# Kernel optimization log

Hardware: AMD Instinct MI355X
Metric: run time of the kernel (lower is better)

The kernel has to match this reference:

```python
import jax, jax.numpy as jnp
import numpy as np

# dims: batch B, seq T, model C, expert hidden H, num experts E, top-k K
B, T, C, H, E, K = 4, 1024, 1024, 1024, 8, 2


def _swiglu(x):
    a, b = jnp.split(x, 2, axis=-1)
    return jax.nn.silu(a) * b


def setup_inputs() -> dict:
    key = jax.random.key(0)
    ks = jax.random.split(key, 6)
    s = 0.02
    x = jax.random.normal(ks[0], (B, T, C), jnp.float32)
    # weights stored [in, out] (transpose of torch Linear layout; same math y = x @ W)
    w_shared_in = jax.random.normal(ks[1], (C, 2 * H), jnp.float32) * s
    w_shared_out = jax.random.normal(ks[2], (H, C), jnp.float32) * s
    w1_shared = jax.random.normal(ks[3], (C, 2 * H), jnp.float32) * s
    w2 = jax.random.normal(ks[4], (E, H, C), jnp.float32) * s  # stacked routed_w2
    w_gate = jax.random.normal(ks[5], (C, E), jnp.float32) * s
    gate_bias = jnp.zeros((E,), jnp.float32)  # buffer, updated only in training
    return {
        "x": x,
        "w_shared_in": w_shared_in,
        "w_shared_out": w_shared_out,
        "w1_shared": w1_shared,
        "w2": w2,
        "w_gate": w_gate,
        "gate_bias": gate_bias,
    }


def reference(x, w_shared_in, w_shared_out, w1_shared, w2, w_gate, gate_bias):
    Bx, Tx, Cx = x.shape
    S = Bx * Tx
    fx = x.reshape(S, Cx)  # [S, C]

    # shared expert: SwiGLU MLP
    shared_out = _swiglu(fx @ w_shared_in) @ w_shared_out  # [S, C]

    # router: softmax(top-k) over biased logits
    logits = fx @ w_gate + gate_bias  # [S, E]
    probs = jax.nn.softmax(logits, axis=-1)
    top_val, top_idx = jax.lax.top_k(probs, K)  # [S, K]

    # dense dispatch-weight matrix [S, E] (zero where expert not selected)
    wdense = jnp.zeros((S, E), probs.dtype).at[
        jnp.arange(S)[:, None], top_idx
    ].add(top_val)

    # routed experts share w1_shared, so the SwiGLU hidden is identical for all
    # experts; compute it once for every token, then apply per-expert w2.
    hid = _swiglu(fx @ w1_shared)  # [S, H]
    routed_out = jnp.zeros_like(shared_out)
    for e in range(E):  # small fixed expert count
        routed_out = routed_out + wdense[:, e:e + 1] * (hid @ w2[e])

    return (shared_out + routed_out).reshape(Bx, Tx, Cx)
```

## Files before the change

kernel.cpp:

```cpp
#include <hip/hip_runtime.h>
#include <stdint.h>

typedef __attribute__((ext_vector_type(4))) float f32x4;
typedef __attribute__((ext_vector_type(8))) short s16x8;

static constexpr int S_TOK = 4096;
static constexpr int CDIM  = 1024;
static constexpr int HDIM  = 1024;
static constexpr int H2    = 2048;
static constexpr int NEXP  = 8;

#define MAXRT2 40

__device__ __forceinline__ unsigned short f2bf(float f) {
  union { float f; uint32_t u; } c; c.f = f;
  uint32_t u = c.u;
  u += 0x7fffu + ((u >> 16) & 1u);
  return (unsigned short)(u >> 16);
}

__device__ __forceinline__ float bf2f(unsigned short u) {
  return __uint_as_float(((uint32_t)u) << 16);
}

__device__ __forceinline__ void gload16(const void* g, void* l) {
  __builtin_amdgcn_global_load_lds(
      (const __attribute__((address_space(1))) void*)g,
      (__attribute__((address_space(3))) void*)l, 16, 0, 0);
}

__global__ void cast_bf16_kernel(const float* __restrict__ src,
                                 unsigned short* __restrict__ dst, int n4) {
  int i = blockIdx.x * blockDim.x + threadIdx.x;
  const int st = gridDim.x * blockDim.x;
  for (; i < n4; i += st) {
    float4 v = reinterpret_cast<const float4*>(src)[i];
    ushort4 o;
    o.x = f2bf(v.x); o.y = f2bf(v.y); o.z = f2bf(v.z); o.w = f2bf(v.w);
    reinterpret_cast<ushort4*>(dst)[i] = o;
  }
}

__global__ void wprep_in_kernel(const float* __restrict__ wsi, const float* __restrict__ w1s,
                                unsigned short* __restrict__ dst) {
  __shared__ float t[32][33];
  const float* src = blockIdx.z ? w1s : wsi;
  const int halfoff = blockIdx.z ? 2048 : 0;
  const int r0 = blockIdx.y * 32;
  const int c0 = blockIdx.x * 32;
  const int tid = threadIdx.x;
#pragma unroll
  for (int i = 0; i < 4; ++i) {
    int idx = tid + i * 256;
    int r = idx >> 5, c = idx & 31;
    t[r][c] = src[(size_t)(r0 + r) * H2 + c0 + c];
  }
  __syncthreads();
#pragma unroll
  for (int i = 0; i < 4; ++i) {
    int idx = tid + i * 256;
    int r = idx >> 5, c = idx & 31;
    const int ccol = c0 + r;
    const int part = ccol >> 10, h = ccol & 1023;
    const int drow = halfoff + (h & 15) + ((h >> 4) << 5) + (part << 4);
    dst[(size_t)drow * CDIM + r0 + c] = f2bf(t[c][r]);
  }
}

__global__ void transpose_cast_kernel(const float* __restrict__ src,
                                      unsigned short* __restrict__ dst,
                                      int R, int Cc) {
  __shared__ float t[32][33];
  const size_t zoff = (size_t)blockIdx.z * R * Cc;
  src += zoff; dst += zoff;
  const int r0 = blockIdx.y * 32;
  const int c0 = blockIdx.x * 32;
  const int tid = threadIdx.x;
#pragma unroll
  for (int i = 0; i < 4; ++i) {
    int idx = tid + i * 256;
    int r = idx >> 5, c = idx & 31;
    t[r][c] = src[(size_t)(r0 + r) * Cc + c0 + c];
  }
  __syncthreads();
#pragma unroll
  for (int i = 0; i < 4; ++i) {
    int idx = tid + i * 256;
    int r = idx >> 5, c = idx & 31;
    dst[(size_t)(c0 + r) * R + r0 + c] = f2bf(t[c][r]);
  }
}

__global__ void router_kernel(const float* __restrict__ x, const float* __restrict__ wg,
                              const float* __restrict__ gb,
                              int2* __restrict__ ti_e, float2* __restrict__ ti_w) {
  const int l = threadIdx.x & 63;
  const int wid = threadIdx.x >> 6;
  const int s = blockIdx.x * 4 + wid;
  const float* xr = x + (size_t)s * CDIM;
  float acc[NEXP];
#pragma unroll
  for (int e = 0; e < NEXP; ++e) acc[e] = 0.f;
  for (int c = l; c < CDIM; c += 64) {
    float xv = xr[c];
    const float* wr_ = wg + (size_t)c * NEXP;
#pragma unroll
    for (int e = 0; e < NEXP; ++e) acc[e] += xv * wr_[e];
  }
#pragma unroll
  for (int e = 0; e < NEXP; ++e) {
#pragma unroll
    for (int off = 32; off > 0; off >>= 1) acc[e] += __shfl_xor(acc[e], off);
    acc[e] += gb[e];
  }
  float m = acc[0];
#pragma unroll
  for (int e = 1; e < NEXP; ++e) m = fmaxf(m, acc[e]);
  float ex[NEXP], sum = 0.f;
#pragma unroll
  for (int e = 0; e < NEXP; ++e) { ex[e] = __expf(acc[e] - m); sum += ex[e]; }
  int i0 = 0;
#pragma unroll
  for (int e = 1; e < NEXP; ++e) if (acc[e] > acc[i0]) i0 = e;
  int i1 = (i0 == 0) ? 1 : 0;
#pragma unroll
  for (int e = 0; e < NEXP; ++e) {
    if (e == i0) continue;
    if (acc[e] > acc[i1]) i1 = e;
  }
  if (l == 0) {
    const float inv = 1.f / sum;
    ti_e[s] = make_int2(i0, i1);
    ti_w[s] = make_float2(ex[i0] * inv, ex[i1] * inv);
  }
}

__global__ __launch_bounds__(1024) void build_kernel(
    const int2* __restrict__ ti_e,
    int* __restrict__ cnt, int* __restrict__ offs,
    int* __restrict__ gidx, int2* __restrict__ ti_slot) {
  __shared__ int gcnt[64][NEXP];
  __shared__ int gbase[64][NEXP];
  __shared__ int eoff[NEXP];
  const int tid = threadIdx.x;
  const int wid = tid >> 6, lane = tid & 63;

  for (int p = 0; p < 4; ++p) {
    const int g = p * 16 + wid;
    const int2 e = ti_e[g * 64 + lane];
#pragma unroll
    for (int ex = 0; ex < NEXP; ++ex) {
      uint64_t b0 = __ballot(e.x == ex);
      uint64_t b1 = __ballot(e.y == ex);
      if (lane == 0) gcnt[g][ex] = __popcll(b0) + __popcll(b1);
    }
  }
  __syncthreads();
  if (tid < NEXP) {
    const int ex = tid;
    int a = 0;
    for (int g = 0; g < 64; ++g) { gbase[g][ex] = a; a += gcnt[g][ex]; }
    eoff[ex] = a;
  }
  __syncthreads();
  if (tid == 0) {
    int a = 0;
#pragma unroll
    for (int ex = 0; ex < NEXP; ++ex) {
      const int c = eoff[ex];
      offs[ex] = a; cnt[ex] = c; eoff[ex] = a; a += c;
    }
    offs[NEXP] = a;
  }
  __syncthreads();
  for (int p = 0; p < 4; ++p) {
    const int g = p * 16 + wid;
    const int s = g * 64 + lane;
    const int2 e = ti_e[s];
    const uint64_t below = (lane == 0) ? 0ull : (~0ull >> (64 - lane));
    const uint64_t beloweq = below | (1ull << lane);
    int slot0 = 0, slot1 = 0;
#pragma unroll
    for (int ex = 0; ex < NEXP; ++ex) {
      uint64_t b0 = __ballot(e.x == ex);
      uint64_t b1 = __ballot(e.y == ex);
      const int base = gbase[g][ex];
      if (e.x == ex) slot0 = base + __popcll(b0 & below) + __popcll(b1 & below);
      if (e.y == ex) slot1 = base + __popcll(b0 & beloweq) + __popcll(b1 & below);
    }
    ti_slot[s] = make_int2(slot0, slot1);
    gidx[eoff[e.x] + slot0] = s;
    gidx[eoff[e.y] + slot1] = s;
  }
}


template<bool LAST>
__device__ __forceinline__ void iter8(
    const unsigned short* a00, const unsigned short* a01,
    const unsigned short* a10, const unsigned short* a11,
    const unsigned short* b00, const unsigned short* b01,
    const unsigned short* b10, const unsigned short* b11,
    unsigned short* SA, unsigned short* SB,
    int e, int t8, int awb, int bwb, int ak0, int ak1,
    f32x4 (&acc)[8][4]) {
  const int o = e + 1;
  s16x8 a[4][2], bl[2][2], bh[2][2];

#define LD_A4(d, F0) { _Pragma("unroll") for (int f_ = 0; f_ < 4; ++f_) { \
    const unsigned short* p_ = SA + (d) * 16384 + awb + ((F0) + f_) * 1024; \
    a[f_][0] = *reinterpret_cast<const s16x8*>(p_ + ak0); \
    a[f_][1] = *reinterpret_cast<const s16x8*>(p_ + ak1); } }
#define LD_B2(d, bb, N0) { _Pragma("unroll") for (int n_ = 0; n_ < 2; ++n_) { \
    const unsigned short* p_ = SB + (d) * 16384 + bwb + ((N0) + n_) * 1024; \
    bb[n_][0] = *reinterpret_cast<const s16x8*>(p_ + ak0); \
    bb[n_][1] = *reinterpret_cast<const s16x8*>(p_ + ak1); } }
#define STG2(S, d, h, p0, p1, kt) { \
    gload16((p0) + (size_t)(kt) * 64, (S) + (d) * 16384 + (h) * 8192 + t8); \
    gload16((p1) + (size_t)(kt) * 64, (S) + (d) * 16384 + (h) * 8192 + 4096 + t8); }
#define QUAD(F0, bb, N0) { _Pragma("unroll") for (int k_ = 0; k_ < 2; ++k_) \
    { _Pragma("unroll") for (int f_ = 0; f_ < 4; ++f_) \
      { _Pragma("unroll") for (int n_ = 0; n_ < 2; ++n_) \
        acc[(F0) + f_][(N0) + n_] = __builtin_amdgcn_mfma_f32_16x16x32_bf16( \
            a[f_][k_], bb[n_][k_], acc[(F0) + f_][(N0) + n_], 0, 0, 0); } } }
#define PH_MID() { asm volatile("" ::: "memory"); __builtin_amdgcn_s_barrier(); \
    asm volatile("s_waitcnt lgkmcnt(0)" ::: "memory"); __builtin_amdgcn_s_setprio(1); }
#define PH_END() { __builtin_amdgcn_s_setprio(0); asm volatile("" ::: "memory"); \
    __builtin_amdgcn_s_barrier(); asm volatile("" ::: "memory"); }

  LD_A4(0, 0) LD_B2(0, bl, 0)
  STG2(SA, 1, 0, a00, a01, o) STG2(SA, 1, 1, a10, a11, o)
  PH_MID() QUAD(0, bl, 0) PH_END()
  LD_B2(0, bh, 2)
  PH_MID() QUAD(0, bh, 2) PH_END()
  LD_A4(0, 4)
  if (!LAST) STG2(SB, 0, 0, b00, b01, e + 2)
  PH_MID() QUAD(4, bh, 2) PH_END()
  if (!LAST) {
    STG2(SB, 0, 1, b10, b11, e + 2)
    asm volatile("s_waitcnt vmcnt(4)" ::: "memory");
  } else {
    asm volatile("s_waitcnt vmcnt(0)" ::: "memory");
  }
  PH_MID() QUAD(4, bl, 0) PH_END()
  LD_A4(1, 0) LD_B2(1, bl, 0)
  if (!LAST) STG2(SA, 0, 0, a00, a01, e + 2)
  PH_MID() QUAD(0, bl, 0) PH_END()
  LD_B2(1, bh, 2)
  if (!LAST) STG2(SA, 0, 1, a10, a11, e + 2)
  PH_MID() QUAD(0, bh, 2) PH_END()
  LD_A4(1, 4)
  if (!LAST) STG2(SB, 1, 0, b00, b01, o + 2)
  PH_MID() QUAD(4, bh, 2) PH_END()
  if (!LAST) {
    STG2(SB, 1, 1, b10, b11, o + 2)
    asm volatile("s_waitcnt vmcnt(4)" ::: "memory");
  }
  PH_MID() QUAD(4, bl, 0) PH_END()

#undef LD_A4
#undef LD_B2
#undef STG2
#undef QUAD
#undef PH_MID
#undef PH_END
}

__device__ __forceinline__ void prologue8(
    const unsigned short* a00, const unsigned short* a01,
    const unsigned short* a10, const unsigned short* a11,
    const unsigned short* b00, const unsigned short* b01,
    const unsigned short* b10, const unsigned short* b11,
    unsigned short* SA, unsigned short* SB, int t8) {
  gload16(a00, SA + t8);                gload16(a01, SA + 4096 + t8);
  gload16(a10, SA + 8192 + t8);         gload16(a11, SA + 8192 + 4096 + t8);
  gload16(b00, SB + t8);                gload16(b01, SB + 4096 + t8);
  gload16(b10, SB + 8192 + t8);         gload16(b11, SB + 8192 + 4096 + t8);
  gload16(b00 + 64, SB + 16384 + t8);   gload16(b01 + 64, SB + 16384 + 4096 + t8);
  gload16(b10 + 64, SB + 16384 + 8192 + t8);
  gload16(b11 + 64, SB + 16384 + 8192 + 4096 + t8);
  asm volatile("s_waitcnt vmcnt(4)" ::: "memory");
  asm volatile("" ::: "memory");
  __builtin_amdgcn_s_barrier();
  asm volatile("" ::: "memory");
}

__global__ __launch_bounds__(512, 2) void gemm1_kernel(
    const unsigned short* __restrict__ xb, const unsigned short* __restrict__ w12i,
    unsigned short* __restrict__ Hs, unsigned short* __restrict__ Hr) {
  __shared__ unsigned short SA[32768];
  __shared__ unsigned short SB[32768];
  const int tid = threadIdx.x;
  const int l = tid & 63, wid = tid >> 6;
  const int wm = wid >> 2, wn = wid & 3;
  const int lr = l & 15;
  const int awb = wm * 8192 + lr * 64;
  const int bwb = wn * 4096 + lr * 64;
  const int ak0 = (((l >> 4) << 3)) ^ ((l & 7) << 3);
  const int ak1 = 32 ^ ak0;
  const int hw = blockIdx.y * gridDim.x + blockIdx.x;
  const int logical = (hw & 7) * 32 + (hw >> 3);
  const int m0 = (logical >> 4) * 256;
  const int n0 = (logical & 15) * 256;
  const int srow = tid >> 3;
  const int scol = (((tid & 7) ^ (srow & 7)) << 3);
  const int t8 = tid * 8;
  f32x4 acc[8][4] = {};
  const unsigned short* a00 = xb + (size_t)(m0 + srow) * CDIM + scol;
  const unsigned short* a01 = a00 + (size_t)64 * CDIM;
  const unsigned short* a10 = a00 + (size_t)128 * CDIM;
  const unsigned short* a11 = a00 + (size_t)192 * CDIM;
  const unsigned short* b00 = w12i + (size_t)(n0 + srow) * CDIM + scol;
  const unsigned short* b01 = b00 + (size_t)64 * CDIM;
  const unsigned short* b10 = b00 + (size_t)128 * CDIM;
  const unsigned short* b11 = b00 + (size_t)192 * CDIM;

  prologue8(a00, a01, a10, a11, b00, b01, b10, b11, SA, SB, t8);
  for (int it = 0; it < 7; ++it)
    iter8<false>(a00, a01, a10, a11, b00, b01, b10, b11, SA, SB, 2 * it,
                 t8, awb, bwb, ak0, ak1, acc);
  iter8<true>(a00, a01, a10, a11, b00, b01, b10, b11, SA, SB, 14,
              t8, awb, bwb, ak0, ak1, acc);

  unsigned short* Hbuf = (n0 < 2048) ? Hs : Hr;
  const int rb = m0 + wm * 128 + ((l >> 4) << 2);
  const int hbase = ((n0 & 2047) >> 1) + wn * 32;
#pragma unroll
  for (int fm = 0; fm < 8; ++fm)
#pragma unroll
    for (int j = 0; j < 2; ++j)
#pragma unroll
      for (int r = 0; r < 4; ++r) {
        float av = acc[fm][2 * j][r];
        float bv = acc[fm][2 * j + 1][r];
        float hv = (av / (1.f + __expf(-av))) * bv;
        Hbuf[(size_t)(rb + fm * 16 + r) * HDIM + hbase + j * 16 + lr] = f2bf(hv);
      }
}

__global__ __launch_bounds__(512, 2) void gemm2_kernel(
    const unsigned short* __restrict__ Hs, const unsigned short* __restrict__ Hr,
    const unsigned short* __restrict__ wso_t, const unsigned short* __restrict__ w2t,
    const int* __restrict__ cnt, const int* __restrict__ offs, const int* __restrict__ gidx,
    unsigned short* __restrict__ Dout, unsigned short* __restrict__ Eout) {
  __shared__ unsigned short SA[32768];
  __shared__ unsigned short SB[32768];
  const int tid = threadIdx.x;
  const int l = tid & 63, wid = tid >> 6;
  const int wm = wid >> 2, wn = wid & 3;
  const int lr = l & 15;
  const int awb = wm * 8192 + lr * 64;
  const int bwb = wn * 4096 + lr * 64;
  const int ak0 = (((l >> 4) << 3)) ^ ((l & 7) << 3);
  const int ak1 = 32 ^ ak0;
  const int hw = blockIdx.y * gridDim.x + blockIdx.x;
  const int logical = (hw & 7) * 28 + (hw >> 3);
  const int gx = logical >> 2;
  const int n0 = (logical & 3) * 256;
  const int srow = tid >> 3;
  const int scol = (((tid & 7) ^ (srow & 7)) << 3);
  const int t8 = tid * 8;
  f32x4 acc[8][4] = {};

  const unsigned short *a00, *a01, *a10, *a11, *b00, *b01, *b10, *b11;
  int e = 0, cnte = 0, mt = 0, base = 0;
  const bool dense = (gx < 16);
  if (dense) {
    const int m0 = gx * 256;
    a00 = Hs + (size_t)(m0 + srow) * HDIM + scol;
    a01 = a00 + (size_t)64 * HDIM;
    a10 = a00 + (size_t)128 * HDIM;
    a11 = a00 + (size_t)192 * HDIM;
    b00 = wso_t + (size_t)(n0 + srow) * HDIM + scol;
    b01 = b00 + (size_t)64 * HDIM;
    b10 = b00 + (size_t)128 * HDIM;
    b11 = b00 + (size_t)192 * HDIM;
  } else {
    int t = gx - 16;
    bool found = false;
#pragma unroll
    for (int ee = 0; ee < NEXP; ++ee) {
      int c = cnt[ee];
      int nt = (c + 255) >> 8;
      if (!found) {
        if (t < nt) { e = ee; cnte = c; found = true; }
        else t -= nt;
      }
    }
    if (!found) return;
    mt = t;
    base = offs[e];
    const int r0 = mt * 256 + srow;
    const int t0 = gidx[base + min(r0,       cnte - 1)];
    const int t1 = gidx[base + min(r0 + 64,  cnte - 1)];
    const int t2 = gidx[base + min(r0 + 128, cnte - 1)];
    const int t3 = gidx[base + min(r0 + 192, cnte - 1)];
    a00 = Hr + (size_t)t0 * HDIM + scol;
    a01 = Hr + (size_t)t1 * HDIM + scol;
    a10 = Hr + (size_t)t2 * HDIM + scol;
    a11 = Hr + (size_t)t3 * HDIM + scol;
    b00 = w2t + (size_t)e * CDIM * HDIM + (size_t)(n0 + srow) * HDIM + scol;
    b01 = b00 + (size_t)64 * HDIM;
    b10 = b00 + (size_t)128 * HDIM;
    b11 = b00 + (size_t)192 * HDIM;
  }

  prologue8(a00, a01, a10, a11, b00, b01, b10, b11, SA, SB, t8);
  for (int it = 0; it < 7; ++it)
    iter8<false>(a00, a01, a10, a11, b00, b01, b10, b11, SA, SB, 2 * it,
                 t8, awb, bwb, ak0, ak1, acc);
  iter8<true>(a00, a01, a10, a11, b00, b01, b10, b11, SA, SB, 14,
              t8, awb, bwb, ak0, ak1, acc);

  const int rloc0 = wm * 128 + ((l >> 4) << 2);
  const int cb = n0 + wn * 64 + lr;
  if (dense) {
    const int rb = gx * 256 + rloc0;
#pragma unroll
    for (int fm = 0; fm < 8; ++fm)
#pragma unroll
      for (int fn = 0; fn < 4; ++fn)
#pragma unroll
        for (int r = 0; r < 4; ++r)
          Dout[(size_t)(rb + fm * 16 + r) * CDIM + cb + fn * 16] = f2bf(acc[fm][fn][r]);
  } else {
#pragma unroll
    for (int fm = 0; fm < 8; ++fm)
#pragma unroll
      for (int fn = 0; fn < 4; ++fn)
#pragma unroll
        for (int r = 0; r < 4; ++r) {
          const int rloc = mt * 256 + rloc0 + fm * 16 + r;
          if (rloc < cnte)
            Eout[(size_t)(base + rloc) * CDIM + cb + fn * 16] = f2bf(acc[fm][fn][r]);
        }
  }
}

__global__ void scatter_kernel(float* __restrict__ out, const unsigned short* __restrict__ Dout,
                               const unsigned short* __restrict__ Eout,
                               const int2* __restrict__ ti_e, const int2* __restrict__ ti_slot,
                               const float2* __restrict__ ti_w, const int* __restrict__ offs) {
  const int total = S_TOK * (CDIM / 8);
  int i = blockIdx.x * blockDim.x + threadIdx.x;
  const int st = gridDim.x * blockDim.x;
  for (; i < total; i += st) {
    const int s = i >> 7;
    const int j = (i & 127) << 3;
    const int2 e = ti_e[s];
    const int2 sl = ti_slot[s];
    const float2 wv = ti_w[s];
    const int p0 = offs[e.x] + sl.x;
    const int p1 = offs[e.y] + sl.y;
    const ushort4* d0 = reinterpret_cast<const ushort4*>(Dout + (size_t)s * CDIM + j);
    const ushort4* e0 = reinterpret_cast<const ushort4*>(Eout + (size_t)p0 * CDIM + j);
    const ushort4* e1 = reinterpret_cast<const ushort4*>(Eout + (size_t)p1 * CDIM + j);
    float* op = out + (size_t)s * CDIM + j;
#pragma unroll
    for (int q = 0; q < 2; ++q) {
      ushort4 dd = d0[q], a = e0[q], b = e1[q];
      float4 o;
      o.x = bf2f(dd.x) + wv.x * bf2f(a.x) + wv.y * bf2f(b.x);
      o.y = bf2f(dd.y) + wv.x * bf2f(a.y) + wv.y * bf2f(b.y);
      o.z = bf2f(dd.z) + wv.x * bf2f(a.z) + wv.y * bf2f(b.z);
      o.w = bf2f(dd.w) + wv.x * bf2f(a.w) + wv.y * bf2f(b.w);
      reinterpret_cast<float4*>(op)[q] = o;
    }
  }
}

extern "C" void kernel_launch(void* const* d_in, const int* in_sizes, int n_in,
                              void* d_out, int out_size, void* d_ws, size_t ws_size,
                              hipStream_t stream) {
  (void)in_sizes; (void)n_in; (void)out_size; (void)ws_size;
  const float* x   = (const float*)d_in[0];
  const float* wsi = (const float*)d_in[1];
  const float* wso = (const float*)d_in[2];
  const float* w1s = (const float*)d_in[3];
  const float* w2  = (const float*)d_in[4];
  const float* wg  = (const float*)d_in[5];
  const float* gb  = (const float*)d_in[6];
  float* out = (float*)d_out;

  char* w = (char*)d_ws;
  auto alloc = [&](size_t bytes) {
    char* p = w; w += (bytes + 255) & ~(size_t)255; return p;
  };
  unsigned short* xb    = (unsigned short*)alloc((size_t)S_TOK * CDIM * 2);
  unsigned short* w12i  = (unsigned short*)alloc((size_t)2 * H2 * CDIM * 2);
  unsigned short* wso_t = (unsigned short*)alloc((size_t)CDIM * HDIM * 2);
  unsigned short* w2t   = (unsigned short*)alloc((size_t)NEXP * CDIM * HDIM * 2);
  unsigned short* Hs    = (unsigned short*)alloc((size_t)S_TOK * HDIM * 2);
  unsigned short* Hr    = (unsigned short*)alloc((size_t)S_TOK * HDIM * 2);
  unsigned short* Dout  = (unsigned short*)alloc((size_t)S_TOK * CDIM * 2);
  unsigned short* Eout  = (unsigned short*)alloc((size_t)2 * S_TOK * CDIM * 2);
  int2*   ti_e   = (int2*)alloc((size_t)S_TOK * 8);
  int2*   ti_slot= (int2*)alloc((size_t)S_TOK * 8);
  float2* ti_w   = (float2*)alloc((size_t)S_TOK * 8);
  int*    cnt    = (int*)alloc(64);
  int*    offs   = (int*)alloc(64);
  int*    gidx   = (int*)alloc((size_t)2 * S_TOK * 4);

  router_kernel<<<S_TOK / 4, 256, 0, stream>>>(x, wg, gb, ti_e, ti_w);
  build_kernel<<<1, 1024, 0, stream>>>(ti_e, cnt, offs, gidx, ti_slot);

  cast_bf16_kernel<<<2048, 256, 0, stream>>>(x, xb, S_TOK * CDIM / 4);
  wprep_in_kernel<<<dim3(H2 / 32, CDIM / 32, 2), 256, 0, stream>>>(wsi, w1s, w12i);
  transpose_cast_kernel<<<dim3(CDIM / 32, HDIM / 32, 1), 256, 0, stream>>>(wso, wso_t, HDIM, CDIM);
  transpose_cast_kernel<<<dim3(CDIM / 32, HDIM / 32, NEXP), 256, 0, stream>>>(w2, w2t, HDIM, CDIM);

  gemm1_kernel<<<dim3(16, 16), 512, 0, stream>>>(xb, w12i, Hs, Hr);

  gemm2_kernel<<<dim3(16 + MAXRT2, CDIM / 256), 512, 0, stream>>>(
      Hs, Hr, wso_t, w2t, cnt, offs, gidx, Dout, Eout);

  scatter_kernel<<<2048, 256, 0, stream>>>(out, Dout, Eout, ti_e, ti_slot, ti_w, offs);
}
```

Before: 122.4 us.

## Replace pipelined 256x256 gemm1 with simple 128x128 single-buffered tile kernel

Replaces the software-pipelined, double-buffered gemm1 (256x256 tiles, 512 threads, swizzled LDS) with a simpler 128x128 tile kernel using 256 threads, BK=32, one LDS buffer and barriers around each k-step. The grid grows from 256 to 1024 blocks to raise occupancy and wave count on the many CUs. In exchange it loses the global-to-LDS prefetch overlap and the LDS swizzle, so it adds bank conflicts and exposed load latency on every k-step.

```diff
diff --git a/kernel.cpp b/kernel.cpp
--- a/kernel.cpp
+++ b/kernel.cpp
@@ -10,6 +10,7 @@
 static constexpr int H2    = 2048;
 static constexpr int NEXP  = 8;
 
+#define BK1 32
 #define MAXRT2 40
 
 __device__ __forceinline__ unsigned short f2bf(float f) {
@@ -194,6 +195,61 @@
   }
 }
 
+__global__ __launch_bounds__(256, 4) void gemm1_kernel(
+    const unsigned short* __restrict__ xb, const unsigned short* __restrict__ w12i,
+    unsigned short* __restrict__ Hs, unsigned short* __restrict__ Hr) {
+  __shared__ unsigned short As[128 * BK1];
+  __shared__ unsigned short Bs[128 * BK1];
+  const int tid = threadIdx.x;
+  const int l = tid & 63, wid = tid >> 6;
+  const int wr = wid >> 1, wc = wid & 1;
+  const int lr = l & 15, lk = (l >> 4) << 3;
+  const int hw = blockIdx.y * gridDim.x + blockIdx.x;
+  const int logical = (hw & 7) * 128 + (hw >> 3);
+  const int m0 = (logical >> 5) * 128;
+  const int n0 = (logical & 31) * 128;
+  f32x4 acc[4][4] = {};
+  const unsigned short* ga0 = xb + (size_t)(m0 + (tid >> 2)) * CDIM + ((tid & 3) << 3);
+  const unsigned short* ga1 = ga0 + (size_t)64 * CDIM;
+  const unsigned short* gb0 = w12i + (size_t)(n0 + (tid >> 2)) * CDIM + ((tid & 3) << 3);
+  const unsigned short* gb1 = gb0 + (size_t)64 * CDIM;
+
+  for (int k0 = 0; k0 < 1024; k0 += BK1) {
+    gload16(ga0 + k0, As + tid * 8);
+    gload16(ga1 + k0, As + 2048 + tid * 8);
+    gload16(gb0 + k0, Bs + tid * 8);
+    gload16(gb1 + k0, Bs + 2048 + tid * 8);
+    __syncthreads();
+    s16x8 a[4], b[4];
+#pragma unroll
+    for (int fm = 0; fm < 4; ++fm)
+      a[fm] = *reinterpret_cast<const s16x8*>(As + (wr * 64 + fm * 16 + lr) * BK1 + lk);
+#pragma unroll
+    for (int fn = 0; fn < 4; ++fn)
+      b[fn] = *reinterpret_cast<const s16x8*>(Bs + (wc * 64 + fn * 16 + lr) * BK1 + lk);
+#pragma unroll
+    for (int fm = 0; fm < 4; ++fm)
+#pragma unroll
+      for (int fn = 0; fn < 4; ++fn)
+        acc[fm][fn] = __builtin_amdgcn_mfma_f32_16x16x32_bf16(a[fm], b[fn], acc[fm][fn], 0, 0, 0);
+    __syncthreads();
+  }
+
+  unsigned short* Hbuf = (n0 < 2048) ? Hs : Hr;
+  const int rb = m0 + wr * 64 + ((l >> 4) << 2);
+  const int hb0 = ((n0 & 2047) >> 1) + wc * 32;
+#pragma unroll
+  for (int fm = 0; fm < 4; ++fm)
+#pragma unroll
+    for (int j = 0; j < 2; ++j)
+#pragma unroll
+      for (int r = 0; r < 4; ++r) {
+        float a = acc[fm][2 * j][r];
+        float b = acc[fm][2 * j + 1][r];
+        float hv = (a / (1.f + __expf(-a))) * b;
+        Hbuf[(size_t)(rb + fm * 16 + r) * HDIM + hb0 + j * 16 + lr] = f2bf(hv);
+      }
+}
 
 template<bool LAST>
 __device__ __forceinline__ void iter8(
@@ -283,59 +339,6 @@
   asm volatile("" ::: "memory");
   __builtin_amdgcn_s_barrier();
   asm volatile("" ::: "memory");
-}
-
-__global__ __launch_bounds__(512, 2) void gemm1_kernel(
-    const unsigned short* __restrict__ xb, const unsigned short* __restrict__ w12i,
-    unsigned short* __restrict__ Hs, unsigned short* __restrict__ Hr) {
-  __shared__ unsigned short SA[32768];
-  __shared__ unsigned short SB[32768];
-  const int tid = threadIdx.x;
-  const int l = tid & 63, wid = tid >> 6;
-  const int wm = wid >> 2, wn = wid & 3;
-  const int lr = l & 15;
-  const int awb = wm * 8192 + lr * 64;
-  const int bwb = wn * 4096 + lr * 64;
-  const int ak0 = (((l >> 4) << 3)) ^ ((l & 7) << 3);
-  const int ak1 = 32 ^ ak0;
-  const int hw = blockIdx.y * gridDim.x + blockIdx.x;
-  const int logical = (hw & 7) * 32 + (hw >> 3);
-  const int m0 = (logical >> 4) * 256;
-  const int n0 = (logical & 15) * 256;
-  const int srow = tid >> 3;
-  const int scol = (((tid & 7) ^ (srow & 7)) << 3);
-  const int t8 = tid * 8;
-  f32x4 acc[8][4] = {};
-  const unsigned short* a00 = xb + (size_t)(m0 + srow) * CDIM + scol;
-  const unsigned short* a01 = a00 + (size_t)64 * CDIM;
-  const unsigned short* a10 = a00 + (size_t)128 * CDIM;
-  const unsigned short* a11 = a00 + (size_t)192 * CDIM;
-  const unsigned short* b00 = w12i + (size_t)(n0 + srow) * CDIM + scol;
-  const unsigned short* b01 = b00 + (size_t)64 * CDIM;
-  const unsigned short* b10 = b00 + (size_t)128 * CDIM;
-  const unsigned short* b11 = b00 + (size_t)192 * CDIM;
-
-  prologue8(a00, a01, a10, a11, b00, b01, b10, b11, SA, SB, t8);
-  for (int it = 0; it < 7; ++it)
-    iter8<false>(a00, a01, a10, a11, b00, b01, b10, b11, SA, SB, 2 * it,
-                 t8, awb, bwb, ak0, ak1, acc);
-  iter8<true>(a00, a01, a10, a11, b00, b01, b10, b11, SA, SB, 14,
-              t8, awb, bwb, ak0, ak1, acc);
-
-  unsigned short* Hbuf = (n0 < 2048) ? Hs : Hr;
-  const int rb = m0 + wm * 128 + ((l >> 4) << 2);
-  const int hbase = ((n0 & 2047) >> 1) + wn * 32;
-#pragma unroll
-  for (int fm = 0; fm < 8; ++fm)
-#pragma unroll
-    for (int j = 0; j < 2; ++j)
-#pragma unroll
-      for (int r = 0; r < 4; ++r) {
-        float av = acc[fm][2 * j][r];
-        float bv = acc[fm][2 * j + 1][r];
-        float hv = (av / (1.f + __expf(-av))) * bv;
-        Hbuf[(size_t)(rb + fm * 16 + r) * HDIM + hbase + j * 16 + lr] = f2bf(hv);
-      }
 }
 
 __global__ __launch_bounds__(512, 2) void gemm2_kernel(
@@ -509,7 +512,7 @@
   transpose_cast_kernel<<<dim3(CDIM / 32, HDIM / 32, 1), 256, 0, stream>>>(wso, wso_t, HDIM, CDIM);
   transpose_cast_kernel<<<dim3(CDIM / 32, HDIM / 32, NEXP), 256, 0, stream>>>(w2, w2t, HDIM, CDIM);
 
-  gemm1_kernel<<<dim3(16, 16), 512, 0, stream>>>(xb, w12i, Hs, Hr);
+  gemm1_kernel<<<dim3(32, 32), 256, 0, stream>>>(xb, w12i, Hs, Hr);
 
   gemm2_kernel<<<dim3(16 + MAXRT2, CDIM / 256), 512, 0, stream>>>(
       Hs, Hr, wso_t, w2t, cnt, offs, gidx, Dout, Eout);
```

Measured after the change: 127.1 us. +3.8%, slower.
